# Kernel tuning notes

Measured on AMD Instinct MI355X. Metric: run time of the kernel, lower is better.

## Reference

```python
import jax, jax.numpy as jnp
import numpy as np

ALPHA, BETA, GAMMA = 1.0, 1.0, 0.7
WIN = 11
C1 = 0.01 ** 2
C2 = 0.03 ** 2


def get_sobel_kernels(n1=1, n2=2, n3=2):
    a = np.asarray
    Sx = a([[[-n1, 0, n1], [-n2, 0, n2], [-n1, 0, n1]],
            [[-n2, 0, n2], [-n3 * n2, 0, n3 * n2], [-n2, 0, n2]],
            [[-n1, 0, n1], [-n2, 0, n2], [-n1, 0, n1]]])
    Sy = a([[[-n1, -n2, -n1], [0, 0, 0], [n1, n2, n1]],
            [[-n2, -n3 * n2, -n2], [0, 0, 0], [n2, n3 * n2, n2]],
            [[-n1, -n2, -n1], [0, 0, 0], [n1, n2, n1]]])
    Sz = a([[[-n1, -n2, -n1], [-n2, -n3 * n2, -n2], [-n1, -n2, -n1]],
            [[0, 0, 0], [0, 0, 0], [0, 0, 0]],
            [[n1, n2, n1], [n2, n3 * n2, n2], [n1, n2, n1]]])
    Sd11 = a([[[0, n1, n2], [-n1, 0, n1], [-n2, -n1, 0]],
              [[0, n2, n2 * n3], [-n2, 0, n2], [-n2 * n3, -n2, 0]],
              [[0, n1, n2], [-n1, 0, n1], [-n2, -n1, 0]]])
    Sd12 = a([[[-n2, -n1, 0], [-n1, 0, n1], [0, n1, n2]],
              [[-n2 * n3, -n2, 0], [-n2, 0, n2], [0, n2, n2 * n3]],
              [[-n2, -n1, 0], [-n1, 0, n1], [0, n1, n2]]])
    Sd21 = Sd11.T
    Sd22 = Sd12.T
    Sd31 = a([-S.T for S in Sd11.T])
    Sd32 = a([S.T for S in Sd12.T])
    return np.stack([Sx, Sy, Sz, Sd11, Sd12, Sd21, Sd22, Sd31, Sd32]).astype(np.float32)

# (9,1,3,3,3) fused sobel bank -- single grouped conv instead of 9 launches
SOBEL_W = jnp.asarray(get_sobel_kernels()[:, None])


def _gauss1d():
    g = jnp.exp(-(jnp.arange(WIN, dtype=jnp.float32) - WIN // 2) ** 2 / (2 * 1.5 ** 2))
    return g / g.sum()

G1D = _gauss1d()


def conv3d(x, w):
    return jax.lax.conv_general_dilated(
        x, w, window_strides=(1, 1, 1), padding='SAME',
        dimension_numbers=('NCDHW', 'OIDHW', 'NCDHW'))


def gauss_filter(x):
    # separable 11-tap gaussian along D, H, W (== full 11^3 window, zero-padded SAME)
    x = conv3d(x, G1D.reshape(1, 1, WIN, 1, 1))
    x = conv3d(x, G1D.reshape(1, 1, 1, WIN, 1))
    x = conv3d(x, G1D.reshape(1, 1, 1, 1, WIN))
    return x


def edge_map(img):
    # GradEdge3D.__call__ with a=1, C=1
    B, C, D, H, W = img.shape
    xp = jnp.pad(img, ((0, 0), (0, 0), (1, 1), (1, 1), (1, 1)), mode='reflect')
    g = conv3d(xp, SOBEL_W)                       # (B, 9, D+2, H+2, W+2)
    gm = jnp.sqrt(jnp.sum((g + 1e-6) ** 2 + 1e-6, axis=1))  # (B, D+2, H+2, W+2)
    gm = gm[:, 1:-1, 1:-1, 1:-1]
    norm = (gm - gm.min()) / (gm.max() - gm.min() + 1e-6)
    return norm.reshape(B, 1, D, H, W)


def ssim_value(pred, target):
    mu_p = gauss_filter(pred)
    mu_t = gauss_filter(target)
    mu_p2, mu_t2, mu_pt = mu_p ** 2, mu_t ** 2, mu_p * mu_t
    sig_p = gauss_filter(pred * pred) - mu_p2
    sig_t = gauss_filter(target * target) - mu_t2
    sig_pt = gauss_filter(pred * target) - mu_pt
    ssim_map = ((2 * mu_pt + C1) * (2 * sig_pt + C2)) / ((mu_p2 + mu_t2 + C1) * (sig_p + sig_t + C2))
    return 1.0 - ssim_map.mean()


def setup_inputs() -> dict:
    key = jax.random.key(0)
    k1, k2 = jax.random.split(key)
    shape = (2, 1, 128, 128, 128)
    return {
        'pred': jax.random.uniform(k1, shape, dtype=jnp.float32),
        'target': jax.random.uniform(k2, shape, dtype=jnp.float32),
    }


def reference(pred, target):
    loss_mse = jnp.mean((pred - target) ** 2)
    loss_ssim = ssim_value(pred, target)
    # GMELoss3D: lam_errors=[(1.0, L1Loss())], reduction='sum'
    loss_gme = 1e-6 + jnp.mean(jnp.abs(edge_map(pred) - edge_map(target)))
    total = ALPHA * loss_mse + BETA * loss_ssim + GAMMA * loss_gme
    return (total, loss_mse, loss_ssim, loss_gme)
```

## Files before the change

### kernel.cpp

```cpp
#include <hip/hip_runtime.h>


#define VOL 4194304
#define HV  2097152

typedef _Float16 h2 __attribute__((ext_vector_type(2)));
typedef _Float16 h8 __attribute__((ext_vector_type(8)));

constexpr float GW[11] = {
    0.00102838f, 0.00759876f, 0.03600077f, 0.10936070f, 0.21300554f,
    0.26601173f,
    0.21300554f, 0.10936070f, 0.03600077f, 0.00759876f, 0.00102838f};


__global__ __launch_bounds__(256) void k_init(double* dbl, unsigned int* ui) {
  const int tid = threadIdx.x + (blockIdx.x << 8);
  if (tid < 1536) dbl[tid] = 0.0;
  if (tid < 4096) ui[tid] = (tid < 2048) ? 0x7F800000u : 0u;
}

__global__ __launch_bounds__(256) void k_wblur_mse(
    const float* __restrict__ p, const float* __restrict__ t,
    _Float16* __restrict__ A, double* __restrict__ mseB) {
  __shared__ float pr[2][138];
  __shared__ float tr[2][138];
  __shared__ float red[256];
  const int tid = threadIdx.x;
  const int rl = tid >> 7;
  const int x  = tid & 127;
  const int rowBase = blockIdx.x << 4;
  if (x < 5)    { pr[rl][x] = 0.f;      tr[rl][x] = 0.f; }
  if (x >= 123) { pr[rl][10 + x] = 0.f; tr[rl][10 + x] = 0.f; }
  float pv = p[((rowBase + rl) << 7) + x];
  float tv = t[((rowBase + rl) << 7) + x];
  float msel = 0.f;
  for (int it = 0; it < 8; ++it) {
    const int row  = rowBase + (it << 1) + rl;
    const int base = row << 7;
    pr[rl][5 + x] = pv; tr[rl][5 + x] = tv;
    __syncthreads();
    float pvN = 0.f, tvN = 0.f;
    if (it < 7) {
      const int baseN = (row + 2) << 7;
      pvN = p[baseN + x]; tvN = t[baseN + x];
    }
    float ap = 0.f, at = 0.f, app = 0.f, att = 0.f, apt = 0.f;
#pragma unroll
    for (int k = 0; k < 11; ++k) {
      const float w = GW[k];
      const float a = pr[rl][x + k];
      const float b = tr[rl][x + k];
      ap += w * a; at += w * b;
      app += w * a * a; att += w * b * b; apt += w * a * b;
    }
    const int idx = base + x;
    A[idx]           = (_Float16)ap;
    A[VOL + idx]     = (_Float16)at;
    A[2 * VOL + idx] = (_Float16)app;
    A[3 * VOL + idx] = (_Float16)att;
    A[4 * VOL + idx] = (_Float16)apt;
    const float d = pv - tv;
    msel += d * d;
    __syncthreads();
    pv = pvN; tv = tvN;
  }
  red[tid] = msel;
  __syncthreads();
  for (int s = 128; s > 0; s >>= 1) {
    if (tid < s) red[tid] += red[tid + s];
    __syncthreads();
  }
  if (tid == 0) atomicAdd(&mseB[(blockIdx.x & 63) << 3], (double)red[0]);
}

__global__ __launch_bounds__(256) void k_blur_y(
    const _Float16* __restrict__ A, _Float16* __restrict__ B) {
  __shared__ h8 s[5][26][16];
  const int tid = threadIdx.x;
  const int z  = blockIdx.x;
  const int y0 = blockIdx.y << 4;
  const int b8 = blockIdx.z << 18;
  const h8* __restrict__ Ah = (const h8*)A;
  h8* __restrict__ Bh = (h8*)B;
  const int slice8 = b8 + (z << 11);
  for (int q = 0; q < 5; ++q) {
    const h8* __restrict__ Aq = Ah + (q << 19) + slice8;
    for (int l = tid; l < 416; l += 256) {
      const int row = l >> 4, xc = l & 15;
      const int y = y0 - 5 + row;
      h8 v{};
      if ((unsigned)y < 128u) v = Aq[(y << 4) + xc];
      s[q][row][xc] = v;
    }
  }
  __syncthreads();
  const int xc = tid & 15;
  const int yo = tid >> 4;
  const int wbase = slice8 + ((y0 + yo) << 4) + xc;
#pragma unroll
  for (int q = 0; q < 5; ++q) {
    h8 acc{};
#pragma unroll
    for (int k = 0; k < 11; ++k) {
      const _Float16 w = (_Float16)GW[k];
      acc += w * s[q][yo + k][xc];
    }
    Bh[(q << 19) + wbase] = acc;
  }
}

__global__ __launch_bounds__(256) void k_zblur_ssim(
    const _Float16* __restrict__ B, double* __restrict__ ssimB) {
  __shared__ h8 s[5][26][16];
  __shared__ float red[256];
  const int tid = threadIdx.x;
  const int y  = blockIdx.x;
  const int z0 = blockIdx.y << 4;
  const int b8 = blockIdx.z << 18;
  const h8* __restrict__ Bh = (const h8*)B;
  const int col8 = b8 + (y << 4);
  for (int q = 0; q < 5; ++q) {
    const h8* __restrict__ Bq = Bh + (q << 19) + col8;
    for (int l = tid; l < 416; l += 256) {
      const int row = l >> 4, xc = l & 15;
      const int zz = z0 - 5 + row;
      h8 v{};
      if ((unsigned)zz < 128u) v = Bq[(zz << 11) + xc];
      s[q][row][xc] = v;
    }
  }
  __syncthreads();
  const int xc = tid & 15;
  const int zo = tid >> 4;
  h8 m[5];
#pragma unroll
  for (int q = 0; q < 5; ++q) {
    h8 acc{};
#pragma unroll
    for (int k = 0; k < 11; ++k) {
      const _Float16 w = (_Float16)GW[k];
      acc += w * s[q][zo + k][xc];
    }
    m[q] = acc;
  }
  float lsum = 0.f;
#pragma unroll
  for (int j = 0; j < 8; ++j) {
    const float mp  = (float)m[0][j];
    const float mt  = (float)m[1][j];
    const float epp = (float)m[2][j];
    const float ett = (float)m[3][j];
    const float ept = (float)m[4][j];
    const float mp2 = mp * mp, mt2 = mt * mt, mpt = mp * mt;
    const float num = (2.f * mpt + 1e-4f) * (2.f * (ept - mpt) + 9e-4f);
    const float den = (mp2 + mt2 + 1e-4f) * ((epp - mp2) + (ett - mt2) + 9e-4f);
    lsum += num / den;
  }
  red[tid] = lsum;
  __syncthreads();
  for (int st = 128; st > 0; st >>= 1) {
    if (tid < st) red[tid] += red[tid + st];
    __syncthreads();
  }
  if (tid == 0) {
    const int bin = (blockIdx.x + (blockIdx.y << 3) + blockIdx.z) & 63;
    atomicAdd(&ssimB[bin << 3], (double)red[0]);
  }
}

__global__ __launch_bounds__(256) void k_sobel(
    const float* __restrict__ p, const float* __restrict__ t,
    _Float16* __restrict__ gmP, _Float16* __restrict__ gmT,
    unsigned int* __restrict__ ui) {
  __shared__ float sb[972];
  __shared__ float rmin[256];
  __shared__ float rmax[256];
  const int tid = threadIdx.x;
  const int tx = tid & 15;
  const int ty = tid >> 4;
  const int x0 = blockIdx.x << 4;
  const int y0 = blockIdx.y << 4;
  const int vol = blockIdx.z >> 3;
  const int b   = (blockIdx.z >> 2) & 1;
  const int z0  = (blockIdx.z & 3) << 5;
  const float* __restrict__ img = vol ? t : p;
  _Float16* __restrict__ gm = vol ? gmT : gmP;
  const int vb = b << 21;

  const int l1 = tid;
  const int ly1 = l1 / 18, lx1 = l1 % 18;
  int gy1 = y0 - 1 + ly1; gy1 = gy1 < 0 ? 1 : (gy1 > 127 ? 126 : gy1);
  int gx1 = x0 - 1 + lx1; gx1 = gx1 < 0 ? 1 : (gx1 > 127 ? 126 : gx1);
  const int off1 = (gy1 << 7) + gx1;
  const int l2 = tid + 256;
  const int ly2 = l2 / 18, lx2 = l2 % 18;
  int gy2 = y0 - 1 + ly2; gy2 = gy2 < 0 ? 1 : (gy2 > 127 ? 126 : gy2);
  int gx2 = x0 - 1 + lx2; gx2 = gx2 < 0 ? 1 : (gx2 > 127 ? 126 : gx2);
  const int off2 = (gy2 << 7) + gx2;
  const bool has2 = (tid < 68);
  const int rb = ty * 18 + tx;
  const int gbase = vb + (z0 << 14) + ((y0 + ty) << 7) + (x0 + tx);

  float Y0[7], Y1[7], Y2[7];
  float rv1 = 0.f, rv2 = 0.f;
  float lmin = 3.4e38f, lmax = 0.f;

#define LOADR(ZS) {                                                         \
    const int zc_ = (ZS) > 127 ? 126 : (ZS);                                \
    const int za_ = vb + (zc_ << 14);                                       \
    rv1 = img[za_ + off1];                                                  \
    if (has2) rv2 = img[za_ + off2]; }

#define WRITELDS(BOFF) {                                                    \
    sb[(BOFF) + l1] = rv1;                                                  \
    if (has2) sb[(BOFF) + l2] = rv2; }

#define COMPY(P) {                                                          \
    const int o_ = (P) * 324 + rb;                                          \
    const float r00 = sb[o_],      r01 = sb[o_ + 1],  r02 = sb[o_ + 2];     \
    const float r10 = sb[o_ + 18], r11 = sb[o_ + 19], r12 = sb[o_ + 20];    \
    const float r20 = sb[o_ + 36], r21 = sb[o_ + 37], r22 = sb[o_ + 38];    \
    const float dx0 = r02 - r00, dx1 = r12 - r10, dx2 = r22 - r20;          \
    const float ux0 = r00 + r01 + r02, ux1 = r10 + r11 + r12,               \
                ux2 = r20 + r21 + r22;                                      \
    const float sx0 = ux0 + r01, sx1 = ux1 + r11, sx2 = ux2 + r21;          \
    Y##P[1] = dx0 + dx1 + dx2;                                    \
    Y##P[0] = Y##P[1] + dx1;                                      \
    Y##P[2] = sx2 - sx0;                                          \
    Y##P[4] = sx0 + sx1 + sx2;                                    \
    Y##P[3] = Y##P[4] + sx1;                                      \
    Y##P[5] = ux2 - ux0;                                          \
    Y##P[6] = (ux0 + ux2) + 2.f * ux1; }

#define EMIT(I, P0, P1, P2) {                                               \
    const float E_ = Y##P0[0] + Y##P1[0] + Y##P2[0];                        \
    const float g1 = E_ + Y##P1[0];                                         \
    const float tA = Y##P0[1] + Y##P1[1] + Y##P2[1];                        \
    const float A_ = tA + Y##P1[1];                                         \
    const float D_ = Y##P0[2] + Y##P1[2] + Y##P2[2];                        \
    const float g2 = D_ + Y##P1[2];                                         \
    const float g3 = Y##P2[3] - Y##P0[3];                                   \
    const float C_ = Y##P2[4] - Y##P0[4];                                   \
    const float B_ = (Y##P0[5] + Y##P2[5]) + 2.f * Y##P1[5];                \
    const float F_ = Y##P2[6] - Y##P0[6];                                   \
    const float g4 = A_ - B_, g5 = A_ + B_;                                 \
    const float g6 = C_ - D_, g7 = C_ + D_;                                 \
    const float g8 = E_ - F_, g9 = E_ + F_;                                 \
    float ss_ = 9e-6f, t_;                                                  \
    t_ = g1 + 1e-6f; ss_ = fmaf(t_, t_, ss_);                               \
    t_ = g2 + 1e-6f; ss_ = fmaf(t_, t_, ss_);                               \
    t_ = g3 + 1e-6f; ss_ = fmaf(t_, t_, ss_);                               \
    t_ = g4 + 1e-6f; ss_ = fmaf(t_, t_, ss_);                               \
    t_ = g5 + 1e-6f; ss_ = fmaf(t_, t_, ss_);                               \
    t_ = g6 + 1e-6f; ss_ = fmaf(t_, t_, ss_);                               \
    t_ = g7 + 1e-6f; ss_ = fmaf(t_, t_, ss_);                               \
    t_ = g8 + 1e-6f; ss_ = fmaf(t_, t_, ss_);                               \
    t_ = g9 + 1e-6f; ss_ = fmaf(t_, t_, ss_);                               \
    const _Float16 gh = (_Float16)sqrtf(ss_);                               \
    gm[gbase + ((I) << 14)] = gh;                                           \
    const float gq = (float)gh;                                             \
    lmin = fminf(lmin, gq); lmax = fmaxf(lmax, gq); }

#define BODY(I, P0, P1, P2) {                                               \
    WRITELDS((P2) * 324);                                                   \
    LOADR(z0 + (I) + 2);                                                    \
    __syncthreads();                                                        \
    COMPY(P2);                                                              \
    EMIT(I, P0, P1, P2); }

  {
    const int zp = (z0 == 0) ? 1 : (z0 - 1);
    LOADR(zp);  WRITELDS(0);
    LOADR(z0);  WRITELDS(324);
    __syncthreads();
    COMPY(0);
    COMPY(1);
    LOADR(z0 + 1);
  }
  for (int ii = 0; ii < 30; ii += 3) {
    BODY(ii,     0, 1, 2);
    BODY(ii + 1, 1, 2, 0);
    BODY(ii + 2, 2, 0, 1);
  }
  BODY(30, 0, 1, 2);
  BODY(31, 1, 2, 0);

#undef BODY
#undef EMIT
#undef COMPY
#undef WRITELDS
#undef LOADR

  rmin[tid] = lmin; rmax[tid] = lmax;
  __syncthreads();
  for (int st = 128; st > 0; st >>= 1) {
    if (tid < st) {
      rmin[tid] = fminf(rmin[tid], rmin[tid + st]);
      rmax[tid] = fmaxf(rmax[tid], rmax[tid + st]);
    }
    __syncthreads();
  }
  if (tid == 0) {
    const int bin = (blockIdx.x + (blockIdx.y << 3) + (blockIdx.z << 6)) & 63;
    atomicMin(&ui[vol * 1024 + (bin << 4)], __float_as_uint(rmin[0]));
    atomicMax(&ui[2048 + vol * 1024 + (bin << 4)], __float_as_uint(rmax[0]));
  }
}

__global__ __launch_bounds__(256) void k_edge_diff(
    const _Float16* __restrict__ gmP, const _Float16* __restrict__ gmT,
    const unsigned int* __restrict__ ui, double* __restrict__ absB) {
  float mnp = 3.4e38f, mnt = 3.4e38f, mxp = 0.f, mxt = 0.f;
  for (int j = 0; j < 64; ++j) {
    mnp = fminf(mnp, __uint_as_float(ui[j << 4]));
    mnt = fminf(mnt, __uint_as_float(ui[1024 + (j << 4)]));
    mxp = fmaxf(mxp, __uint_as_float(ui[2048 + (j << 4)]));
    mxt = fmaxf(mxt, __uint_as_float(ui[3072 + (j << 4)]));
  }
  const float scp = 1.f / (mxp - mnp + 1e-6f);
  const float sct = 1.f / (mxt - mnt + 1e-6f);
  const h8* __restrict__ gp = (const h8*)gmP;
  const h8* __restrict__ gt = (const h8*)gmT;
  float lsum = 0.f;
  const int base = blockIdx.x << 9;
#pragma unroll
  for (int i = 0; i < 2; ++i) {
    const int idx = base + (i << 8) + threadIdx.x;
    const h8 a = gp[idx];
    const h8 b = gt[idx];
#pragma unroll
    for (int j = 0; j < 8; ++j)
      lsum += fabsf(((float)a[j] - mnp) * scp - ((float)b[j] - mnt) * sct);
  }
  __shared__ float red[256];
  red[threadIdx.x] = lsum;
  __syncthreads();
  for (int s = 128; s > 0; s >>= 1) {
    if (threadIdx.x < s) red[threadIdx.x] += red[threadIdx.x + s];
    __syncthreads();
  }
  if (threadIdx.x == 0)
    atomicAdd(&absB[(blockIdx.x & 63) << 3], (double)red[0]);
}

__global__ void k_final(const double* __restrict__ dbl, float* __restrict__ out) {
  if (threadIdx.x == 0 && blockIdx.x == 0) {
    double ms = 0.0, ss = 0.0, ab = 0.0;
    for (int j = 0; j < 64; ++j) {
      ms += dbl[j << 3];
      ss += dbl[512 + (j << 3)];
      ab += dbl[1024 + (j << 3)];
    }
    const double N = 4194304.0;
    const double mse   = ms / N;
    const double ssiml = 1.0 - ss / N;
    const double gme   = 1e-6 + ab / N;
    const double total = mse + ssiml + 0.7 * gme;
    out[0] = (float)total;
    out[1] = (float)mse;
    out[2] = (float)ssiml;
    out[3] = (float)gme;
  }
}

extern "C" void kernel_launch(void* const* d_in, const int* in_sizes, int n_in,
                              void* d_out, int out_size, void* d_ws, size_t ws_size,
                              hipStream_t stream) {
  const float* p = (const float*)d_in[0];
  const float* t = (const float*)d_in[1];
  _Float16* A = (_Float16*)d_ws;
  _Float16* B = A + (size_t)5 * VOL;
  char* accb = (char*)d_ws + (size_t)20 * VOL;
  double* dbl = (double*)accb;
  unsigned int* ui = (unsigned int*)(accb + 12288);
  float* out = (float*)d_out;
  _Float16* gmP = B;
  _Float16* gmT = gmP + VOL;

  k_init<<<16, 256, 0, stream>>>(dbl, ui);
  k_wblur_mse<<<2048, 256, 0, stream>>>(p, t, A, dbl);
  k_blur_y<<<dim3(128, 8, 2), 256, 0, stream>>>(A, B);
  k_zblur_ssim<<<dim3(128, 8, 2), 256, 0, stream>>>(B, dbl + 512);
  k_sobel<<<dim3(8, 8, 16), 256, 0, stream>>>(p, t, gmP, gmT, ui);
  k_edge_diff<<<1024, 256, 0, stream>>>(gmP, gmT, ui, dbl + 1024);
  k_final<<<1, 64, 0, stream>>>(dbl, out);
}
```

Measured before the change: 165.7 us.

## Fold final reduction into edge-diff kernel and vectorize x-blur loads

Removes the separate final launch. The last k_edge_diff block, found through an atomic counter, now reduces the per-block partial sums and writes the outputs. MSE and SSIM partials go to per-block slots instead of atomics into 64 bins. k_wblur_mse now has each thread handle two adjacent columns, using float2 loads, register windows and half2 stores. The aim is to cut launch overhead and atomic contention at the cost of a serial tail in one block.

```diff
diff --git a/kernel.cpp b/kernel.cpp
--- a/kernel.cpp
+++ b/kernel.cpp
@@ -12,55 +12,69 @@
     0.26601173f,
     0.21300554f, 0.10936070f, 0.03600077f, 0.00759876f, 0.00102838f};
 
-
 __global__ __launch_bounds__(256) void k_init(double* dbl, unsigned int* ui) {
   const int tid = threadIdx.x + (blockIdx.x << 8);
-  if (tid < 1536) dbl[tid] = 0.0;
+  if (tid < 512) dbl[4096 + tid] = 0.0;
   if (tid < 4096) ui[tid] = (tid < 2048) ? 0x7F800000u : 0u;
+  if (tid == 4096) ui[4096] = 0u;
 }
 
 __global__ __launch_bounds__(256) void k_wblur_mse(
     const float* __restrict__ p, const float* __restrict__ t,
-    _Float16* __restrict__ A, double* __restrict__ mseB) {
-  __shared__ float pr[2][138];
-  __shared__ float tr[2][138];
+    _Float16* __restrict__ A, double* __restrict__ mseSlot) {
+  __shared__ float pr[4][140];
+  __shared__ float tr[4][140];
   __shared__ float red[256];
   const int tid = threadIdx.x;
-  const int rl = tid >> 7;
-  const int x  = tid & 127;
+  const int rl = tid >> 6;
+  const int xp = tid & 63;
   const int rowBase = blockIdx.x << 4;
-  if (x < 5)    { pr[rl][x] = 0.f;      tr[rl][x] = 0.f; }
-  if (x >= 123) { pr[rl][10 + x] = 0.f; tr[rl][10 + x] = 0.f; }
-  float pv = p[((rowBase + rl) << 7) + x];
-  float tv = t[((rowBase + rl) << 7) + x];
+  if (xp < 5) {
+    pr[rl][xp] = 0.f;       tr[rl][xp] = 0.f;
+    pr[rl][133 + xp] = 0.f; tr[rl][133 + xp] = 0.f;
+  }
+  const float2* __restrict__ p2 = (const float2*)p;
+  const float2* __restrict__ t2 = (const float2*)t;
+  h2* __restrict__ A2 = (h2*)A;
+  float2 pv = p2[((rowBase + rl) << 6) + xp];
+  float2 tv = t2[((rowBase + rl) << 6) + xp];
   float msel = 0.f;
-  for (int it = 0; it < 8; ++it) {
-    const int row  = rowBase + (it << 1) + rl;
-    const int base = row << 7;
-    pr[rl][5 + x] = pv; tr[rl][5 + x] = tv;
-    __syncthreads();
-    float pvN = 0.f, tvN = 0.f;
-    if (it < 7) {
-      const int baseN = (row + 2) << 7;
-      pvN = p[baseN + x]; tvN = t[baseN + x];
-    }
-    float ap = 0.f, at = 0.f, app = 0.f, att = 0.f, apt = 0.f;
+  for (int it = 0; it < 4; ++it) {
+    const int row = rowBase + (it << 2) + rl;
+    pr[rl][5 + (xp << 1)] = pv.x; pr[rl][6 + (xp << 1)] = pv.y;
+    tr[rl][5 + (xp << 1)] = tv.x; tr[rl][6 + (xp << 1)] = tv.y;
+    __syncthreads();
+    float2 pvN = make_float2(0.f, 0.f), tvN = make_float2(0.f, 0.f);
+    if (it < 3) {
+      pvN = p2[((row + 4) << 6) + xp];
+      tvN = t2[((row + 4) << 6) + xp];
+    }
+    float wp[12], wt[12];
+#pragma unroll
+    for (int k = 0; k < 12; ++k) {
+      wp[k] = pr[rl][(xp << 1) + k];
+      wt[k] = tr[rl][(xp << 1) + k];
+    }
+    float ap0=0.f,ap1=0.f,at0=0.f,at1=0.f,app0=0.f,app1=0.f,
+          att0=0.f,att1=0.f,apt0=0.f,apt1=0.f;
 #pragma unroll
     for (int k = 0; k < 11; ++k) {
       const float w = GW[k];
-      const float a = pr[rl][x + k];
-      const float b = tr[rl][x + k];
-      ap += w * a; at += w * b;
-      app += w * a * a; att += w * b * b; apt += w * a * b;
-    }
-    const int idx = base + x;
-    A[idx]           = (_Float16)ap;
-    A[VOL + idx]     = (_Float16)at;
-    A[2 * VOL + idx] = (_Float16)app;
-    A[3 * VOL + idx] = (_Float16)att;
-    A[4 * VOL + idx] = (_Float16)apt;
-    const float d = pv - tv;
-    msel += d * d;
+      const float a0 = wp[k], a1 = wp[k+1], b0 = wt[k], b1 = wt[k+1];
+      ap0 += w*a0; ap1 += w*a1; at0 += w*b0; at1 += w*b1;
+      app0 += w*a0*a0; app1 += w*a1*a1;
+      att0 += w*b0*b0; att1 += w*b1*b1;
+      apt0 += w*a0*b0; apt1 += w*a1*b1;
+    }
+    const int idx2 = (row << 6) + xp;
+    h2 o;
+    o.x=(_Float16)ap0;  o.y=(_Float16)ap1;  A2[idx2] = o;
+    o.x=(_Float16)at0;  o.y=(_Float16)at1;  A2[(VOL>>1) + idx2] = o;
+    o.x=(_Float16)app0; o.y=(_Float16)app1; A2[2*(VOL>>1) + idx2] = o;
+    o.x=(_Float16)att0; o.y=(_Float16)att1; A2[3*(VOL>>1) + idx2] = o;
+    o.x=(_Float16)apt0; o.y=(_Float16)apt1; A2[4*(VOL>>1) + idx2] = o;
+    const float d0 = pv.x - tv.x, d1 = pv.y - tv.y;
+    msel += d0*d0 + d1*d1;
     __syncthreads();
     pv = pvN; tv = tvN;
   }
@@ -70,7 +84,7 @@
     if (tid < s) red[tid] += red[tid + s];
     __syncthreads();
   }
-  if (tid == 0) atomicAdd(&mseB[(blockIdx.x & 63) << 3], (double)red[0]);
+  if (tid == 0) mseSlot[blockIdx.x] = (double)red[0];
 }
 
 __global__ __launch_bounds__(256) void k_blur_y(
@@ -110,7 +124,7 @@
 }
 
 __global__ __launch_bounds__(256) void k_zblur_ssim(
-    const _Float16* __restrict__ B, double* __restrict__ ssimB) {
+    const _Float16* __restrict__ B, double* __restrict__ ssimSlot) {
   __shared__ h8 s[5][26][16];
   __shared__ float red[256];
   const int tid = threadIdx.x;
@@ -162,10 +176,9 @@
     if (tid < st) red[tid] += red[tid + st];
     __syncthreads();
   }
-  if (tid == 0) {
-    const int bin = (blockIdx.x + (blockIdx.y << 3) + blockIdx.z) & 63;
-    atomicAdd(&ssimB[bin << 3], (double)red[0]);
-  }
+  if (tid == 0)
+    ssimSlot[blockIdx.x + (blockIdx.y << 7) + (blockIdx.z << 10)] =
+        (double)red[0];
 }
 
 __global__ __launch_bounds__(256) void k_sobel(
@@ -309,7 +322,9 @@
 
 __global__ __launch_bounds__(256) void k_edge_diff(
     const _Float16* __restrict__ gmP, const _Float16* __restrict__ gmT,
-    const unsigned int* __restrict__ ui, double* __restrict__ absB) {
+    const unsigned int* __restrict__ ui, double* __restrict__ dbl,
+    unsigned int* __restrict__ counter, float* __restrict__ out) {
+  const int tid = threadIdx.x;
   float mnp = 3.4e38f, mnt = 3.4e38f, mxp = 0.f, mxt = 0.f;
   for (int j = 0; j < 64; ++j) {
     mnp = fminf(mnp, __uint_as_float(ui[j << 4]));
@@ -325,7 +340,7 @@
   const int base = blockIdx.x << 9;
 #pragma unroll
   for (int i = 0; i < 2; ++i) {
-    const int idx = base + (i << 8) + threadIdx.x;
+    const int idx = base + (i << 8) + tid;
     const h8 a = gp[idx];
     const h8 b = gt[idx];
 #pragma unroll
@@ -333,28 +348,48 @@
       lsum += fabsf(((float)a[j] - mnp) * scp - ((float)b[j] - mnt) * sct);
   }
   __shared__ float red[256];
-  red[threadIdx.x] = lsum;
+  __shared__ double rd[256];
+  __shared__ unsigned int done;
+  red[tid] = lsum;
   __syncthreads();
   for (int s = 128; s > 0; s >>= 1) {
-    if (threadIdx.x < s) red[threadIdx.x] += red[threadIdx.x + s];
-    __syncthreads();
-  }
-  if (threadIdx.x == 0)
-    atomicAdd(&absB[(blockIdx.x & 63) << 3], (double)red[0]);
-}
-
-__global__ void k_final(const double* __restrict__ dbl, float* __restrict__ out) {
-  if (threadIdx.x == 0 && blockIdx.x == 0) {
-    double ms = 0.0, ss = 0.0, ab = 0.0;
-    for (int j = 0; j < 64; ++j) {
-      ms += dbl[j << 3];
-      ss += dbl[512 + (j << 3)];
-      ab += dbl[1024 + (j << 3)];
-    }
+    if (tid < s) red[tid] += red[tid + s];
+    __syncthreads();
+  }
+  if (tid == 0) {
+    atomicAdd(&dbl[4096 + ((blockIdx.x & 63) << 3)], (double)red[0]);
+    __threadfence();
+    done = atomicAdd(counter, 1u);
+  }
+  __syncthreads();
+  if (done != 1023u) return;
+  __threadfence();
+  double ms = 0.0, ss = 0.0;
+  for (int j = tid; j < 2048; j += 256) ms += dbl[j];
+  for (int j = tid; j < 2048; j += 256) ss += dbl[2048 + j];
+  double ab = (tid < 64) ? dbl[4096 + (tid << 3)] : 0.0;
+  rd[tid] = ms; __syncthreads();
+  for (int s = 128; s > 0; s >>= 1) {
+    if (tid < s) rd[tid] += rd[tid + s];
+    __syncthreads();
+  }
+  const double msT = rd[0]; __syncthreads();
+  rd[tid] = ss; __syncthreads();
+  for (int s = 128; s > 0; s >>= 1) {
+    if (tid < s) rd[tid] += rd[tid + s];
+    __syncthreads();
+  }
+  const double ssT = rd[0]; __syncthreads();
+  rd[tid] = ab; __syncthreads();
+  for (int s = 128; s > 0; s >>= 1) {
+    if (tid < s) rd[tid] += rd[tid + s];
+    __syncthreads();
+  }
+  if (tid == 0) {
     const double N = 4194304.0;
-    const double mse   = ms / N;
-    const double ssiml = 1.0 - ss / N;
-    const double gme   = 1e-6 + ab / N;
+    const double mse   = msT / N;
+    const double ssiml = 1.0 - ssT / N;
+    const double gme   = 1e-6 + rd[0] / N;
     const double total = mse + ssiml + 0.7 * gme;
     out[0] = (float)total;
     out[1] = (float)mse;
@@ -372,16 +407,15 @@
   _Float16* B = A + (size_t)5 * VOL;
   char* accb = (char*)d_ws + (size_t)20 * VOL;
   double* dbl = (double*)accb;
-  unsigned int* ui = (unsigned int*)(accb + 12288);
+  unsigned int* ui = (unsigned int*)(accb + 40960);
   float* out = (float*)d_out;
   _Float16* gmP = B;
   _Float16* gmT = gmP + VOL;
 
-  k_init<<<16, 256, 0, stream>>>(dbl, ui);
+  k_init<<<17, 256, 0, stream>>>(dbl, ui);
   k_wblur_mse<<<2048, 256, 0, stream>>>(p, t, A, dbl);
   k_blur_y<<<dim3(128, 8, 2), 256, 0, stream>>>(A, B);
-  k_zblur_ssim<<<dim3(128, 8, 2), 256, 0, stream>>>(B, dbl + 512);
+  k_zblur_ssim<<<dim3(128, 8, 2), 256, 0, stream>>>(B, dbl + 2048);
   k_sobel<<<dim3(8, 8, 16), 256, 0, stream>>>(p, t, gmP, gmT, ui);
-  k_edge_diff<<<1024, 256, 0, stream>>>(gmP, gmT, ui, dbl + 1024);
-  k_final<<<1, 64, 0, stream>>>(dbl, out);
-}
+  k_edge_diff<<<1024, 256, 0, stream>>>(gmP, gmT, ui, dbl, ui + 4096, out);
+}
```

New measurement: 183.7 us. +10.9%, slower.

## Fuse x-blur, y-blur and MSE into one kernel using shared-memory tiles

Applied to the files above, without the earlier changes.

Merges the x-direction Gaussian blur (with MSE) and the y-direction blur into a single kernel. Each block loads a 26-row fp32 tile of pred and target with y-halo, computes the five x-blurred products into a shared fp16 buffer, then runs the y-blur there and writes only the xy-blurred intermediates. This removes the write and re-read of five full-volume fp16 intermediates and one launch. In exchange it recomputes the x-blur for halo rows (26 rows for every 16 output rows), uses a much larger shared-memory footprint that may lower occupancy, and leaves some threads idle in the x-blur stage.

```diff
diff --git a/kernel.cpp b/kernel.cpp
--- a/kernel.cpp
+++ b/kernel.cpp
@@ -19,93 +19,159 @@
   if (tid < 4096) ui[tid] = (tid < 2048) ? 0x7F800000u : 0u;
 }
 
-__global__ __launch_bounds__(256) void k_wblur_mse(
+__global__ __launch_bounds__(256) void k_xyblur_mse(
     const float* __restrict__ p, const float* __restrict__ t,
-    _Float16* __restrict__ A, double* __restrict__ mseB) {
-  __shared__ float pr[2][138];
-  __shared__ float tr[2][138];
+    _Float16* __restrict__ B, double* __restrict__ mseB) {
+  __shared__ float sp[26][141];
+  __shared__ float st[26][141];
+  __shared__ h8 xb[5][26][16];
   __shared__ float red[256];
   const int tid = threadIdx.x;
-  const int rl = tid >> 7;
-  const int x  = tid & 127;
-  const int rowBase = blockIdx.x << 4;
-  if (x < 5)    { pr[rl][x] = 0.f;      tr[rl][x] = 0.f; }
-  if (x >= 123) { pr[rl][10 + x] = 0.f; tr[rl][10 + x] = 0.f; }
-  float pv = p[((rowBase + rl) << 7) + x];
-  float tv = t[((rowBase + rl) << 7) + x];
+  const int z  = blockIdx.x;
+  const int y0 = blockIdx.y << 4;
+  const int b  = blockIdx.z;
+  const int gb = (b << 21) + (z << 14);
+
+  for (int l = tid; l < 3328; l += 256) {
+    const int r = l >> 7, x = l & 127;
+    const int y = y0 - 5 + r;
+    float pv = 0.f, tv = 0.f;
+    if ((unsigned)y < 128u) {
+      pv = p[gb + (y << 7) + x];
+      tv = t[gb + (y << 7) + x];
+    }
+    sp[r][5 + x] = pv; st[r][5 + x] = tv;
+  }
+  for (int l = tid; l < 260; l += 256) {
+    const int r = l / 10, j = l % 10;
+    const int c = (j < 5) ? j : (128 + j);
+    sp[r][c] = 0.f; st[r][c] = 0.f;
+  }
+  __syncthreads();
+
   float msel = 0.f;
-  for (int it = 0; it < 8; ++it) {
-    const int row  = rowBase + (it << 1) + rl;
-    const int base = row << 7;
-    pr[rl][5 + x] = pv; tr[rl][5 + x] = tv;
-    __syncthreads();
-    float pvN = 0.f, tvN = 0.f;
-    if (it < 7) {
-      const int baseN = (row + 2) << 7;
-      pvN = p[baseN + x]; tvN = t[baseN + x];
-    }
-    float ap = 0.f, at = 0.f, app = 0.f, att = 0.f, apt = 0.f;
-#pragma unroll
-    for (int k = 0; k < 11; ++k) {
-      const float w = GW[k];
-      const float a = pr[rl][x + k];
-      const float b = tr[rl][x + k];
-      ap += w * a; at += w * b;
-      app += w * a * a; att += w * b * b; apt += w * a * b;
-    }
-    const int idx = base + x;
-    A[idx]           = (_Float16)ap;
-    A[VOL + idx]     = (_Float16)at;
-    A[2 * VOL + idx] = (_Float16)app;
-    A[3 * VOL + idx] = (_Float16)att;
-    A[4 * VOL + idx] = (_Float16)apt;
-    const float d = pv - tv;
+#pragma unroll
+  for (int i = 0; i < 8; ++i) {
+    const int l = (i << 8) + tid;
+    const int r = 5 + (l >> 7), x = l & 127;
+    const float d = sp[r][5 + x] - st[r][5 + x];
     msel += d * d;
-    __syncthreads();
-    pv = pvN; tv = tvN;
-  }
+  }
+
+  for (int it = 0; it < 2; ++it) {
+    const int i = tid + (it << 8);
+    if (i < 416) {
+      const int r = i >> 4, oct = i & 15, x0 = oct << 3;
+      float a[18], c[18];
+#pragma unroll
+      for (int j = 0; j < 18; ++j) {
+        a[j] = sp[r][x0 + j];
+        c[j] = st[r][x0 + j];
+      }
+      {
+        float acc[8] = {0.f,0.f,0.f,0.f,0.f,0.f,0.f,0.f};
+#pragma unroll
+        for (int k = 0; k < 11; ++k) {
+          const float w = GW[k];
+#pragma unroll
+          for (int j = 0; j < 8; ++j) acc[j] += w * a[j + k];
+        }
+        h8 v;
+#pragma unroll
+        for (int j = 0; j < 8; ++j) v[j] = (_Float16)acc[j];
+        xb[0][r][oct] = v;
+      }
+      {
+        float acc[8] = {0.f,0.f,0.f,0.f,0.f,0.f,0.f,0.f};
+#pragma unroll
+        for (int k = 0; k < 11; ++k) {
+          const float w = GW[k];
+#pragma unroll
+          for (int j = 0; j < 8; ++j) acc[j] += w * c[j + k];
+        }
+        h8 v;
+#pragma unroll
+        for (int j = 0; j < 8; ++j) v[j] = (_Float16)acc[j];
+        xb[1][r][oct] = v;
+      }
+      {
+        float wnd[18];
+#pragma unroll
+        for (int j = 0; j < 18; ++j) wnd[j] = a[j] * a[j];
+        float acc[8] = {0.f,0.f,0.f,0.f,0.f,0.f,0.f,0.f};
+#pragma unroll
+        for (int k = 0; k < 11; ++k) {
+          const float w = GW[k];
+#pragma unroll
+          for (int j = 0; j < 8; ++j) acc[j] += w * wnd[j + k];
+        }
+        h8 v;
+#pragma unroll
+        for (int j = 0; j < 8; ++j) v[j] = (_Float16)acc[j];
+        xb[2][r][oct] = v;
+      }
+      {
+        float wnd[18];
+#pragma unroll
+        for (int j = 0; j < 18; ++j) wnd[j] = c[j] * c[j];
+        float acc[8] = {0.f,0.f,0.f,0.f,0.f,0.f,0.f,0.f};
+#pragma unroll
+        for (int k = 0; k < 11; ++k) {
+          const float w = GW[k];
+#pragma unroll
+          for (int j = 0; j < 8; ++j) acc[j] += w * wnd[j + k];
+        }
+        h8 v;
+#pragma unroll
+        for (int j = 0; j < 8; ++j) v[j] = (_Float16)acc[j];
+        xb[3][r][oct] = v;
+      }
+      {
+        float wnd[18];
+#pragma unroll
+        for (int j = 0; j < 18; ++j) wnd[j] = a[j] * c[j];
+        float acc[8] = {0.f,0.f,0.f,0.f,0.f,0.f,0.f,0.f};
+#pragma unroll
+        for (int k = 0; k < 11; ++k) {
+          const float w = GW[k];
+#pragma unroll
+          for (int j = 0; j < 8; ++j) acc[j] += w * wnd[j + k];
+        }
+        h8 v;
+#pragma unroll
+        for (int j = 0; j < 8; ++j) v[j] = (_Float16)acc[j];
+        xb[4][r][oct] = v;
+      }
+    }
+  }
+  __syncthreads();
+
+  {
+    h8* __restrict__ Bh = (h8*)B;
+    const int xc = tid & 15;
+    const int yo = tid >> 4;
+    const int wbase = (b << 18) + (z << 11) + ((y0 + yo) << 4) + xc;
+#pragma unroll
+    for (int q = 0; q < 5; ++q) {
+      h8 acc{};
+#pragma unroll
+      for (int k = 0; k < 11; ++k) {
+        const _Float16 w = (_Float16)GW[k];
+        acc += w * xb[q][yo + k][xc];
+      }
+      Bh[(q << 19) + wbase] = acc;
+    }
+  }
+
   red[tid] = msel;
   __syncthreads();
   for (int s = 128; s > 0; s >>= 1) {
     if (tid < s) red[tid] += red[tid + s];
     __syncthreads();
   }
-  if (tid == 0) atomicAdd(&mseB[(blockIdx.x & 63) << 3], (double)red[0]);
-}
-
-__global__ __launch_bounds__(256) void k_blur_y(
-    const _Float16* __restrict__ A, _Float16* __restrict__ B) {
-  __shared__ h8 s[5][26][16];
-  const int tid = threadIdx.x;
-  const int z  = blockIdx.x;
-  const int y0 = blockIdx.y << 4;
-  const int b8 = blockIdx.z << 18;
-  const h8* __restrict__ Ah = (const h8*)A;
-  h8* __restrict__ Bh = (h8*)B;
-  const int slice8 = b8 + (z << 11);
-  for (int q = 0; q < 5; ++q) {
-    const h8* __restrict__ Aq = Ah + (q << 19) + slice8;
-    for (int l = tid; l < 416; l += 256) {
-      const int row = l >> 4, xc = l & 15;
-      const int y = y0 - 5 + row;
-      h8 v{};
-      if ((unsigned)y < 128u) v = Aq[(y << 4) + xc];
-      s[q][row][xc] = v;
-    }
-  }
-  __syncthreads();
-  const int xc = tid & 15;
-  const int yo = tid >> 4;
-  const int wbase = slice8 + ((y0 + yo) << 4) + xc;
-#pragma unroll
-  for (int q = 0; q < 5; ++q) {
-    h8 acc{};
-#pragma unroll
-    for (int k = 0; k < 11; ++k) {
-      const _Float16 w = (_Float16)GW[k];
-      acc += w * s[q][yo + k][xc];
-    }
-    Bh[(q << 19) + wbase] = acc;
+  if (tid == 0) {
+    const int bin = (blockIdx.x + (blockIdx.y << 7) + (blockIdx.z << 10)) & 63;
+    atomicAdd(&mseB[bin << 3], (double)red[0]);
   }
 }
 
@@ -368,18 +434,16 @@
                               hipStream_t stream) {
   const float* p = (const float*)d_in[0];
   const float* t = (const float*)d_in[1];
-  _Float16* A = (_Float16*)d_ws;
-  _Float16* B = A + (size_t)5 * VOL;
+  _Float16* B = (_Float16*)d_ws;
   char* accb = (char*)d_ws + (size_t)20 * VOL;
   double* dbl = (double*)accb;
   unsigned int* ui = (unsigned int*)(accb + 12288);
   float* out = (float*)d_out;
-  _Float16* gmP = B;
+  _Float16* gmP = B + (size_t)5 * VOL;
   _Float16* gmT = gmP + VOL;
 
   k_init<<<16, 256, 0, stream>>>(dbl, ui);
-  k_wblur_mse<<<2048, 256, 0, stream>>>(p, t, A, dbl);
-  k_blur_y<<<dim3(128, 8, 2), 256, 0, stream>>>(A, B);
+  k_xyblur_mse<<<dim3(128, 8, 2), 256, 0, stream>>>(p, t, B, dbl);
   k_zblur_ssim<<<dim3(128, 8, 2), 256, 0, stream>>>(B, dbl + 512);
   k_sobel<<<dim3(8, 8, 16), 256, 0, stream>>>(p, t, gmP, gmT, ui);
   k_edge_diff<<<1024, 256, 0, stream>>>(gmP, gmT, ui, dbl + 1024);
```

Result: slower. 174.2 us (+5.1%).

## Co-schedule independent stages via block-interleaved fused kernels

Applied to the files above, without the earlier changes.

Merges the width blur plus MSE with the Sobel edge stage into one launch, and the y-blur with the edge-difference stage into a second launch. Block indices are split 2:1 between the two bodies. Independent work now overlaps on the GPU and the launch count falls. To make this possible, the gradient-magnitude buffers move to their own workspace region, since they previously aliased buffer B. The cost is a larger union of shared memory per block, which may reduce occupancy, and branch divergence across block roles.

```diff
diff --git a/kernel.cpp b/kernel.cpp
--- a/kernel.cpp
+++ b/kernel.cpp
@@ -19,16 +19,16 @@
   if (tid < 4096) ui[tid] = (tid < 2048) ? 0x7F800000u : 0u;
 }
 
-__global__ __launch_bounds__(256) void k_wblur_mse(
+__device__ __forceinline__ void wblur_body(
     const float* __restrict__ p, const float* __restrict__ t,
-    _Float16* __restrict__ A, double* __restrict__ mseB) {
+    _Float16* __restrict__ A, double* __restrict__ mseB, const int bidx) {
   __shared__ float pr[2][138];
   __shared__ float tr[2][138];
-  __shared__ float red[256];
+  __shared__ float redw[256];
   const int tid = threadIdx.x;
   const int rl = tid >> 7;
   const int x  = tid & 127;
-  const int rowBase = blockIdx.x << 4;
+  const int rowBase = bidx << 4;
   if (x < 5)    { pr[rl][x] = 0.f;      tr[rl][x] = 0.f; }
   if (x >= 123) { pr[rl][10 + x] = 0.f; tr[rl][10 + x] = 0.f; }
   float pv = p[((rowBase + rl) << 7) + x];
@@ -64,125 +64,30 @@
     __syncthreads();
     pv = pvN; tv = tvN;
   }
-  red[tid] = msel;
+  redw[tid] = msel;
   __syncthreads();
   for (int s = 128; s > 0; s >>= 1) {
-    if (tid < s) red[tid] += red[tid + s];
-    __syncthreads();
-  }
-  if (tid == 0) atomicAdd(&mseB[(blockIdx.x & 63) << 3], (double)red[0]);
-}
-
-__global__ __launch_bounds__(256) void k_blur_y(
-    const _Float16* __restrict__ A, _Float16* __restrict__ B) {
-  __shared__ h8 s[5][26][16];
-  const int tid = threadIdx.x;
-  const int z  = blockIdx.x;
-  const int y0 = blockIdx.y << 4;
-  const int b8 = blockIdx.z << 18;
-  const h8* __restrict__ Ah = (const h8*)A;
-  h8* __restrict__ Bh = (h8*)B;
-  const int slice8 = b8 + (z << 11);
-  for (int q = 0; q < 5; ++q) {
-    const h8* __restrict__ Aq = Ah + (q << 19) + slice8;
-    for (int l = tid; l < 416; l += 256) {
-      const int row = l >> 4, xc = l & 15;
-      const int y = y0 - 5 + row;
-      h8 v{};
-      if ((unsigned)y < 128u) v = Aq[(y << 4) + xc];
-      s[q][row][xc] = v;
-    }
-  }
-  __syncthreads();
-  const int xc = tid & 15;
-  const int yo = tid >> 4;
-  const int wbase = slice8 + ((y0 + yo) << 4) + xc;
-#pragma unroll
-  for (int q = 0; q < 5; ++q) {
-    h8 acc{};
-#pragma unroll
-    for (int k = 0; k < 11; ++k) {
-      const _Float16 w = (_Float16)GW[k];
-      acc += w * s[q][yo + k][xc];
-    }
-    Bh[(q << 19) + wbase] = acc;
-  }
-}
-
-__global__ __launch_bounds__(256) void k_zblur_ssim(
-    const _Float16* __restrict__ B, double* __restrict__ ssimB) {
-  __shared__ h8 s[5][26][16];
-  __shared__ float red[256];
-  const int tid = threadIdx.x;
-  const int y  = blockIdx.x;
-  const int z0 = blockIdx.y << 4;
-  const int b8 = blockIdx.z << 18;
-  const h8* __restrict__ Bh = (const h8*)B;
-  const int col8 = b8 + (y << 4);
-  for (int q = 0; q < 5; ++q) {
-    const h8* __restrict__ Bq = Bh + (q << 19) + col8;
-    for (int l = tid; l < 416; l += 256) {
-      const int row = l >> 4, xc = l & 15;
-      const int zz = z0 - 5 + row;
-      h8 v{};
-      if ((unsigned)zz < 128u) v = Bq[(zz << 11) + xc];
-      s[q][row][xc] = v;
-    }
-  }
-  __syncthreads();
-  const int xc = tid & 15;
-  const int zo = tid >> 4;
-  h8 m[5];
-#pragma unroll
-  for (int q = 0; q < 5; ++q) {
-    h8 acc{};
-#pragma unroll
-    for (int k = 0; k < 11; ++k) {
-      const _Float16 w = (_Float16)GW[k];
-      acc += w * s[q][zo + k][xc];
-    }
-    m[q] = acc;
-  }
-  float lsum = 0.f;
-#pragma unroll
-  for (int j = 0; j < 8; ++j) {
-    const float mp  = (float)m[0][j];
-    const float mt  = (float)m[1][j];
-    const float epp = (float)m[2][j];
-    const float ett = (float)m[3][j];
-    const float ept = (float)m[4][j];
-    const float mp2 = mp * mp, mt2 = mt * mt, mpt = mp * mt;
-    const float num = (2.f * mpt + 1e-4f) * (2.f * (ept - mpt) + 9e-4f);
-    const float den = (mp2 + mt2 + 1e-4f) * ((epp - mp2) + (ett - mt2) + 9e-4f);
-    lsum += num / den;
-  }
-  red[tid] = lsum;
-  __syncthreads();
-  for (int st = 128; st > 0; st >>= 1) {
-    if (tid < st) red[tid] += red[tid + st];
-    __syncthreads();
-  }
-  if (tid == 0) {
-    const int bin = (blockIdx.x + (blockIdx.y << 3) + blockIdx.z) & 63;
-    atomicAdd(&ssimB[bin << 3], (double)red[0]);
-  }
-}
-
-__global__ __launch_bounds__(256) void k_sobel(
+    if (tid < s) redw[tid] += redw[tid + s];
+    __syncthreads();
+  }
+  if (tid == 0) atomicAdd(&mseB[(bidx & 63) << 3], (double)redw[0]);
+}
+
+__device__ __forceinline__ void sobel_body(
     const float* __restrict__ p, const float* __restrict__ t,
     _Float16* __restrict__ gmP, _Float16* __restrict__ gmT,
-    unsigned int* __restrict__ ui) {
+    unsigned int* __restrict__ ui, const int bx, const int by, const int bz) {
   __shared__ float sb[972];
   __shared__ float rmin[256];
   __shared__ float rmax[256];
   const int tid = threadIdx.x;
   const int tx = tid & 15;
   const int ty = tid >> 4;
-  const int x0 = blockIdx.x << 4;
-  const int y0 = blockIdx.y << 4;
-  const int vol = blockIdx.z >> 3;
-  const int b   = (blockIdx.z >> 2) & 1;
-  const int z0  = (blockIdx.z & 3) << 5;
+  const int x0 = bx << 4;
+  const int y0 = by << 4;
+  const int vol = bz >> 3;
+  const int b   = (bz >> 2) & 1;
+  const int z0  = (bz & 3) << 5;
   const float* __restrict__ img = vol ? t : p;
   _Float16* __restrict__ gm = vol ? gmT : gmP;
   const int vb = b << 21;
@@ -301,15 +206,53 @@
     __syncthreads();
   }
   if (tid == 0) {
-    const int bin = (blockIdx.x + (blockIdx.y << 3) + (blockIdx.z << 6)) & 63;
+    const int bin = (bx + (by << 3) + (bz << 6)) & 63;
     atomicMin(&ui[vol * 1024 + (bin << 4)], __float_as_uint(rmin[0]));
     atomicMax(&ui[2048 + vol * 1024 + (bin << 4)], __float_as_uint(rmax[0]));
   }
 }
 
-__global__ __launch_bounds__(256) void k_edge_diff(
+__device__ __forceinline__ void blury_body(
+    const _Float16* __restrict__ A, _Float16* __restrict__ B,
+    const int z, const int yseg, const int batch) {
+  __shared__ h8 s[5][26][16];
+  const int tid = threadIdx.x;
+  const int y0 = yseg << 4;
+  const int b8 = batch << 18;
+  const h8* __restrict__ Ah = (const h8*)A;
+  h8* __restrict__ Bh = (h8*)B;
+  const int slice8 = b8 + (z << 11);
+  for (int q = 0; q < 5; ++q) {
+    const h8* __restrict__ Aq = Ah + (q << 19) + slice8;
+    for (int l = tid; l < 416; l += 256) {
+      const int row = l >> 4, xc = l & 15;
+      const int y = y0 - 5 + row;
+      h8 v{};
+      if ((unsigned)y < 128u) v = Aq[(y << 4) + xc];
+      s[q][row][xc] = v;
+    }
+  }
+  __syncthreads();
+  const int xc = tid & 15;
+  const int yo = tid >> 4;
+  const int wbase = slice8 + ((y0 + yo) << 4) + xc;
+#pragma unroll
+  for (int q = 0; q < 5; ++q) {
+    h8 acc{};
+#pragma unroll
+    for (int k = 0; k < 11; ++k) {
+      const _Float16 w = (_Float16)GW[k];
+      acc += w * s[q][yo + k][xc];
+    }
+    Bh[(q << 19) + wbase] = acc;
+  }
+}
+
+__device__ __forceinline__ void edge_body(
     const _Float16* __restrict__ gmP, const _Float16* __restrict__ gmT,
-    const unsigned int* __restrict__ ui, double* __restrict__ absB) {
+    const unsigned int* __restrict__ ui, double* __restrict__ absB,
+    const int bidx) {
+  __shared__ float rede[256];
   float mnp = 3.4e38f, mnt = 3.4e38f, mxp = 0.f, mxt = 0.f;
   for (int j = 0; j < 64; ++j) {
     mnp = fminf(mnp, __uint_as_float(ui[j << 4]));
@@ -322,7 +265,7 @@
   const h8* __restrict__ gp = (const h8*)gmP;
   const h8* __restrict__ gt = (const h8*)gmT;
   float lsum = 0.f;
-  const int base = blockIdx.x << 9;
+  const int base = bidx << 9;
 #pragma unroll
   for (int i = 0; i < 2; ++i) {
     const int idx = base + (i << 8) + threadIdx.x;
@@ -332,15 +275,102 @@
     for (int j = 0; j < 8; ++j)
       lsum += fabsf(((float)a[j] - mnp) * scp - ((float)b[j] - mnt) * sct);
   }
+  rede[threadIdx.x] = lsum;
+  __syncthreads();
+  for (int s = 128; s > 0; s >>= 1) {
+    if (threadIdx.x < s) rede[threadIdx.x] += rede[threadIdx.x + s];
+    __syncthreads();
+  }
+  if (threadIdx.x == 0)
+    atomicAdd(&absB[(bidx & 63) << 3], (double)rede[0]);
+}
+
+__global__ __launch_bounds__(256) void k_fused_a(
+    const float* __restrict__ p, const float* __restrict__ t,
+    _Float16* __restrict__ A, double* __restrict__ mseB,
+    _Float16* __restrict__ gmP, _Float16* __restrict__ gmT,
+    unsigned int* __restrict__ ui) {
+  const int bid = blockIdx.x;
+  const int r3 = bid % 3;
+  if (r3 < 2) {
+    wblur_body(p, t, A, mseB, (bid / 3) * 2 + r3);
+  } else {
+    const int s = bid / 3;
+    sobel_body(p, t, gmP, gmT, ui, s & 7, (s >> 3) & 7, s >> 6);
+  }
+}
+
+__global__ __launch_bounds__(256) void k_fused_b(
+    const _Float16* __restrict__ A, _Float16* __restrict__ B,
+    const _Float16* __restrict__ gmP, const _Float16* __restrict__ gmT,
+    const unsigned int* __restrict__ ui, double* __restrict__ absB) {
+  const int bid = blockIdx.x;
+  const int r3 = bid % 3;
+  if (r3 < 2) {
+    const int idx = (bid / 3) * 2 + r3;
+    blury_body(A, B, idx & 127, (idx >> 7) & 7, idx >> 10);
+  } else {
+    edge_body(gmP, gmT, ui, absB, bid / 3);
+  }
+}
+
+__global__ __launch_bounds__(256) void k_zblur_ssim(
+    const _Float16* __restrict__ B, double* __restrict__ ssimB) {
+  __shared__ h8 s[5][26][16];
   __shared__ float red[256];
-  red[threadIdx.x] = lsum;
-  __syncthreads();
-  for (int s = 128; s > 0; s >>= 1) {
-    if (threadIdx.x < s) red[threadIdx.x] += red[threadIdx.x + s];
-    __syncthreads();
-  }
-  if (threadIdx.x == 0)
-    atomicAdd(&absB[(blockIdx.x & 63) << 3], (double)red[0]);
+  const int tid = threadIdx.x;
+  const int y  = blockIdx.x;
+  const int z0 = blockIdx.y << 4;
+  const int b8 = blockIdx.z << 18;
+  const h8* __restrict__ Bh = (const h8*)B;
+  const int col8 = b8 + (y << 4);
+  for (int q = 0; q < 5; ++q) {
+    const h8* __restrict__ Bq = Bh + (q << 19) + col8;
+    for (int l = tid; l < 416; l += 256) {
+      const int row = l >> 4, xc = l & 15;
+      const int zz = z0 - 5 + row;
+      h8 v{};
+      if ((unsigned)zz < 128u) v = Bq[(zz << 11) + xc];
+      s[q][row][xc] = v;
+    }
+  }
+  __syncthreads();
+  const int xc = tid & 15;
+  const int zo = tid >> 4;
+  h8 m[5];
+#pragma unroll
+  for (int q = 0; q < 5; ++q) {
+    h8 acc{};
+#pragma unroll
+    for (int k = 0; k < 11; ++k) {
+      const _Float16 w = (_Float16)GW[k];
+      acc += w * s[q][zo + k][xc];
+    }
+    m[q] = acc;
+  }
+  float lsum = 0.f;
+#pragma unroll
+  for (int j = 0; j < 8; ++j) {
+    const float mp  = (float)m[0][j];
+    const float mt  = (float)m[1][j];
+    const float epp = (float)m[2][j];
+    const float ett = (float)m[3][j];
+    const float ept = (float)m[4][j];
+    const float mp2 = mp * mp, mt2 = mt * mt, mpt = mp * mt;
+    const float num = (2.f * mpt + 1e-4f) * (2.f * (ept - mpt) + 9e-4f);
+    const float den = (mp2 + mt2 + 1e-4f) * ((epp - mp2) + (ett - mt2) + 9e-4f);
+    lsum += num / den;
+  }
+  red[tid] = lsum;
+  __syncthreads();
+  for (int st = 128; st > 0; st >>= 1) {
+    if (tid < st) red[tid] += red[tid + st];
+    __syncthreads();
+  }
+  if (tid == 0) {
+    const int bin = (blockIdx.x + (blockIdx.y << 3) + blockIdx.z) & 63;
+    atomicAdd(&ssimB[bin << 3], (double)red[0]);
+  }
 }
 
 __global__ void k_final(const double* __restrict__ dbl, float* __restrict__ out) {
@@ -373,15 +403,13 @@
   char* accb = (char*)d_ws + (size_t)20 * VOL;
   double* dbl = (double*)accb;
   unsigned int* ui = (unsigned int*)(accb + 12288);
+  _Float16* gmP = (_Float16*)((char*)d_ws + 88080384);
+  _Float16* gmT = gmP + VOL;
   float* out = (float*)d_out;
-  _Float16* gmP = B;
-  _Float16* gmT = gmP + VOL;
 
   k_init<<<16, 256, 0, stream>>>(dbl, ui);
-  k_wblur_mse<<<2048, 256, 0, stream>>>(p, t, A, dbl);
-  k_blur_y<<<dim3(128, 8, 2), 256, 0, stream>>>(A, B);
+  k_fused_a<<<3072, 256, 0, stream>>>(p, t, A, dbl, gmP, gmT, ui);
+  k_fused_b<<<3072, 256, 0, stream>>>(A, B, gmP, gmT, ui, dbl + 1024);
   k_zblur_ssim<<<dim3(128, 8, 2), 256, 0, stream>>>(B, dbl + 512);
-  k_sobel<<<dim3(8, 8, 16), 256, 0, stream>>>(p, t, gmP, gmT, ui);
-  k_edge_diff<<<1024, 256, 0, stream>>>(gmP, gmT, ui, dbl + 1024);
   k_final<<<1, 64, 0, stream>>>(dbl, out);
 }
```

Measured after the change: 162.6 us. No clear change (-1.8%).
